# Optimization experiments

Hardware: AMD Instinct MI355X
Metric: run time of the kernel (lower is better)

Reference implementation:

```python
import jax, jax.numpy as jnp
import numpy as np


def setup_inputs() -> dict:
    key = jax.random.key(0)
    k1, k2, k3 = jax.random.split(key, 3)
    bs, nvars, T, input_dim = 8, 16, 512, 256
    embed_dim, num_embed, codebook_num = 128, 512, 4
    inp = jax.random.normal(k1, (bs, nvars, T, input_dim), dtype=jnp.float32)
    # xavier_normal_ for (input_dim, embed_dim): std = sqrt(2/(fan_in+fan_out))
    xavier_std = float(np.sqrt(2.0 / (input_dim + embed_dim)))
    projector = jax.random.normal(k2, (input_dim, embed_dim), dtype=jnp.float32) * xavier_std
    codebook = jax.random.normal(k3, (codebook_num, num_embed, embed_dim), dtype=jnp.float32)
    return {"input": inp, "projector": projector, "codebook": codebook}


def reference(input, projector, codebook):
    # project: [b,n,t,input_dim] @ [input_dim,embed_dim] -> [b,n,t,d]
    x = jnp.matmul(input, projector)
    # L2-normalize along last dim (matches torch .norm(dim=-1,keepdim=True) division)
    x = x / jnp.linalg.norm(x, axis=-1, keepdims=True)
    cb = codebook / jnp.linalg.norm(codebook, axis=-1, keepdims=True)
    # cosine similarity: [b,n,t,c,m]
    similarity = jnp.einsum('bntd,cmd->bntcm', x, cb)
    # nearest code per codebook: [b,n,t,c]
    idx = jnp.argmax(similarity, axis=-1)
    return idx
```

## Files before the change

### kernel.cpp

```cpp
#include <hip/hip_runtime.h>
#include <math.h>

#define DIN    256
#define DEMB   128
#define NCB    4
#define MCODES 512
#define NCODE  2048
#define MARGIN 1.5e-4f

using bf16x8 = __attribute__((ext_vector_type(8))) short;
using f32x16 = __attribute__((ext_vector_type(16))) float;

static __device__ __forceinline__ unsigned short f2bf(float f) {
    unsigned u = __float_as_uint(f);
    u += 0x7FFFu + ((u >> 16) & 1u);
    return (unsigned short)(u >> 16);
}
static __device__ __forceinline__ float bf2f(unsigned short h) {
    return __uint_as_float(((unsigned)h) << 16);
}
static __device__ __forceinline__ float4 ld4(const float* p) {
    return *reinterpret_cast<const float4*>(p);
}
static __device__ __forceinline__ void gload_lds16(const void* g, void* l) {
    __builtin_amdgcn_global_load_lds(
        (const __attribute__((address_space(1))) void*)g,
        (__attribute__((address_space(3))) void*)l, 16, 0, 0);
}

__global__ __launch_bounds__(256) void prep_codebook(
        const float* __restrict__ cb, float* __restrict__ cbn,
        unsigned short* __restrict__ cbA) {
    const int w = threadIdx.x >> 6, lane = threadIdx.x & 63;
    const int code = blockIdx.x * 4 + w;
    const float2 v = reinterpret_cast<const float2*>(cb + (size_t)code * DEMB)[lane];
    float ss = v.x * v.x + v.y * v.y;
#pragma unroll
    for (int m = 1; m < 64; m <<= 1) ss += __shfl_xor(ss, m, 64);
    const float rn = 1.0f / sqrtf(ss);
    const float x0 = v.x * rn, x1 = v.y * rn;
    reinterpret_cast<float2*>(cbn + (size_t)code * DEMB)[lane] = make_float2(x0, x1);

    const unsigned short h0 = f2bf(x0), h1 = f2bf(x1);
    const unsigned short l0 = f2bf(x0 - bf2f(h0)), l1 = f2bf(x1 - bf2f(h1));
    const int ct = code >> 5, ci = code & 31;
    const int kt = lane >> 3, g = (lane >> 2) & 1, i = 2 * (lane & 3);
    const size_t base = ((size_t)ct * 1024 + kt * 128 + g * 32 + ci) * 8 + i;
    *reinterpret_cast<ushort2*>(cbA + base)       = make_ushort2(h0, h1);
    *reinterpret_cast<ushort2*>(cbA + base + 512) = make_ushort2(l0, l1);
}

__global__ __launch_bounds__(256) void prep_proj(
        const float* __restrict__ proj, unsigned short* __restrict__ pjA) {
    const int t = blockIdx.x * 256 + threadIdx.x;
    const int ci = t & 31, g = (t >> 5) & 1, kt = (t >> 6) & 15, mt = t >> 10;
    const int m = mt * 32 + ci;
    const size_t base = ((size_t)(mt * 16 + kt) * 3) * 512 + (size_t)(g * 32 + ci) * 8;
#pragma unroll
    for (int i = 0; i < 8; ++i) {
        const float v = proj[(size_t)(kt * 16 + g * 8 + i) * DEMB + m];
        const unsigned short h = f2bf(v);
        const float r1 = v - bf2f(h);
        const unsigned short md = f2bf(r1);
        const float r2 = r1 - bf2f(md);
        pjA[base + i]        = h;
        pjA[base + 512 + i]  = md;
        pjA[base + 1024 + i] = f2bf(r2);
    }
}

__global__ __launch_bounds__(256) void project_mfma(
        const float* __restrict__ inp, const unsigned short* __restrict__ pjA,
        float* __restrict__ xw) {
    const int tid = threadIdx.x;
    const int lane = tid & 63, mt = tid >> 6, kg = lane >> 5;
    const int row = blockIdx.x * 32 + (lane & 31);
    const float* xr = inp + (size_t)row * DIN;
    const unsigned short* pL = pjA + (size_t)lane * 8;

    auto ldin = [&](float4& a, float4& b, int kt) {
        a = ld4(xr + kt * 16 + kg * 8);
        b = ld4(xr + kt * 16 + kg * 8 + 4);
    };

    f32x16 P, Q;
#pragma unroll
    for (int r = 0; r < 16; ++r) { P[r] = 0.0f; Q[r] = 0.0f; }

    auto do_step = [&](const float4& c0, const float4& c1, int kt) {
        const float xs[8] = {c0.x, c0.y, c0.z, c0.w, c1.x, c1.y, c1.z, c1.w};
        bf16x8 Bh, Bm, Bl;
#pragma unroll
        for (int e = 0; e < 8; ++e) {
            const float v = xs[e];
            const unsigned short h = f2bf(v);
            const float r1 = v - bf2f(h);
            const unsigned short md = f2bf(r1);
            const float r2 = r1 - bf2f(md);
            Bh[e] = (short)h; Bm[e] = (short)md; Bl[e] = (short)f2bf(r2);
        }
        const unsigned short* pf = pL + ((size_t)(mt * 16 + kt) * 3) * 512;
        const bf16x8 Ah = *reinterpret_cast<const bf16x8*>(pf);
        const bf16x8 Am = *reinterpret_cast<const bf16x8*>(pf + 512);
        const bf16x8 Al = *reinterpret_cast<const bf16x8*>(pf + 1024);
        P = __builtin_amdgcn_mfma_f32_32x32x16_bf16(Ah, Bh, P, 0, 0, 0);
        Q = __builtin_amdgcn_mfma_f32_32x32x16_bf16(Ah, Bm, Q, 0, 0, 0);
        Q = __builtin_amdgcn_mfma_f32_32x32x16_bf16(Am, Bh, Q, 0, 0, 0);
        Q = __builtin_amdgcn_mfma_f32_32x32x16_bf16(Ah, Bl, Q, 0, 0, 0);
        Q = __builtin_amdgcn_mfma_f32_32x32x16_bf16(Al, Bh, Q, 0, 0, 0);
        Q = __builtin_amdgcn_mfma_f32_32x32x16_bf16(Am, Bm, Q, 0, 0, 0);
    };

    float4 nA0, nA1, nB0, nB1;
    ldin(nA0, nA1, 0);
#pragma unroll 1
    for (int kt = 0; kt < 16; kt += 2) {
        ldin(nB0, nB1, kt + 1);
        do_step(nA0, nA1, kt);
        if (kt + 2 < 16) ldin(nA0, nA1, kt + 2);
        do_step(nB0, nB1, kt + 1);
    }

#pragma unroll
    for (int q = 0; q < 4; ++q) {
        float4 v;
        v.x = P[q * 4 + 0] + Q[q * 4 + 0];
        v.y = P[q * 4 + 1] + Q[q * 4 + 1];
        v.z = P[q * 4 + 2] + Q[q * 4 + 2];
        v.w = P[q * 4 + 3] + Q[q * 4 + 3];
        *reinterpret_cast<float4*>(xw + (size_t)row * DEMB + mt * 32 + q * 8 + kg * 4) = v;
    }
}

__global__ __launch_bounds__(256) void project_kernel(
        const float* __restrict__ inp, const float* __restrict__ proj,
        float* __restrict__ xw) {
    const int tid = threadIdx.x, tx = tid & 31, ty = tid >> 5;
    const int rowBase = blockIdx.x * 64;

    float acc1[8][4];
#pragma unroll
    for (int i = 0; i < 8; ++i)
#pragma unroll
        for (int j = 0; j < 4; ++j) acc1[i][j] = 0.0f;

    const float* inRow0 = inp + (size_t)(rowBase + ty) * DIN;
    const float* pjCol  = proj + tx * 4;

    float4 ivA[8], ivB[8], pjA[4], pjB[4];
    auto load_step = [&](float4 iv[8], float4 pj[4], int kk) {
#pragma unroll
        for (int j = 0; j < 4; ++j) pj[j] = ld4(pjCol + (size_t)(kk + j) * DEMB);
#pragma unroll
        for (int i = 0; i < 8; ++i) iv[i] = ld4(inRow0 + (size_t)(8 * i) * DIN + kk);
    };
    auto fma_step = [&](const float4 iv[8], const float4 pj[4]) {
#pragma unroll
        for (int i = 0; i < 8; ++i) {
            const float* ivp = reinterpret_cast<const float*>(&iv[i]);
#pragma unroll
            for (int j = 0; j < 4; ++j) {
                acc1[i][0] = fmaf(ivp[j], pj[j].x, acc1[i][0]);
                acc1[i][1] = fmaf(ivp[j], pj[j].y, acc1[i][1]);
                acc1[i][2] = fmaf(ivp[j], pj[j].z, acc1[i][2]);
                acc1[i][3] = fmaf(ivp[j], pj[j].w, acc1[i][3]);
            }
        }
    };
    load_step(ivA, pjA, 0);
#pragma unroll 1
    for (int k = 0; k < DIN; k += 8) {
        load_step(ivB, pjB, k + 4);
        fma_step(ivA, pjA);
        if (k + 8 < DIN) load_step(ivA, pjA, k + 8);
        fma_step(ivB, pjB);
    }
#pragma unroll
    for (int i = 0; i < 8; ++i) {
        const int r = rowBase + ty + 8 * i;
        *reinterpret_cast<float4*>(xw + (size_t)r * DEMB + tx * 4) =
            make_float4(acc1[i][0], acc1[i][1], acc1[i][2], acc1[i][3]);
    }
}

__global__ __launch_bounds__(256) void sim_kernel(
        const float* __restrict__ xw,
        const unsigned short* __restrict__ cbA,
        int* __restrict__ out, int* __restrict__ unc_cnt,
        int* __restrict__ unc_list) {
    __shared__ __align__(16) short sA[3][8192];
    const int tid = threadIdx.x;
    const int lane = tid & 63, wv = tid >> 6;
    const int kg = lane >> 5;
    const int cbi = blockIdx.x & 3;
    const int rowBase = (blockIdx.x >> 2) * 128;
    const int row = rowBase + wv * 32 + (lane & 31);

    const short* gA = (const short*)cbA + (size_t)cbi * 16 * 8192;
    auto stage = [&](int buf, int t) {
        const short* g = gA + (size_t)t * 8192 + wv * 2048 + lane * 8;
        short* l = &sA[buf][wv * 2048];
#pragma unroll
        for (int c = 0; c < 4; ++c)
            gload_lds16(g + c * 512, l + c * 512);
    };

    stage(0, 0);
    stage(1, 1);

    bf16x8 Bhi[8], Blo[8];
    {
        const float* xr = xw + (size_t)row * DEMB;
        float4 f0[8], f1[8];
        float ss = 0.0f;
#pragma unroll
        for (int kt = 0; kt < 8; ++kt) {
            f0[kt] = ld4(xr + kt * 16 + kg * 8);
            f1[kt] = ld4(xr + kt * 16 + kg * 8 + 4);
            ss += f0[kt].x * f0[kt].x + f0[kt].y * f0[kt].y +
                  f0[kt].z * f0[kt].z + f0[kt].w * f0[kt].w +
                  f1[kt].x * f1[kt].x + f1[kt].y * f1[kt].y +
                  f1[kt].z * f1[kt].z + f1[kt].w * f1[kt].w;
        }
        ss += __shfl_xor(ss, 32, 64);
        const float rn = 1.0f / sqrtf(ss);
#pragma unroll
        for (int kt = 0; kt < 8; ++kt) {
            const float xs[8] = {f0[kt].x, f0[kt].y, f0[kt].z, f0[kt].w,
                                 f1[kt].x, f1[kt].y, f1[kt].z, f1[kt].w};
            bf16x8 hv, lv;
#pragma unroll
            for (int e = 0; e < 8; ++e) {
                const float xn = xs[e] * rn;
                const unsigned short h = f2bf(xn);
                hv[e] = (short)h;
                lv[e] = (short)f2bf(xn - bf2f(h));
            }
            Bhi[kt] = hv; Blo[kt] = lv;
        }
    }

    f32x16 TWO;
#pragma unroll
    for (int r = 0; r < 16; ++r) TWO[r] = 2.0f;

    f32x16 acc = TWO;
    float t1 = -INFINITY, t2 = -INFINITY; int i1 = 0;

#pragma unroll 1
    for (int g = 0; g < 16; ++g) {
        if (g < 15) asm volatile("s_waitcnt vmcnt(4)" ::: "memory");
        else        asm volatile("s_waitcnt vmcnt(0)" ::: "memory");
        __builtin_amdgcn_s_barrier();
        asm volatile("" ::: "memory");
        if (g + 2 < 16) stage((g + 2) % 3, g + 2);

        const short* pa = &sA[g % 3][lane * 8];
        const f32x16 pAcc = acc;
        __builtin_amdgcn_s_setprio(1);
#pragma unroll
        for (int kt = 0; kt < 8; ++kt) {
            const bf16x8 Ahi = *reinterpret_cast<const bf16x8*>(pa + kt * 1024);
            const bf16x8 Alo = *reinterpret_cast<const bf16x8*>(pa + kt * 1024 + 512);
            acc = __builtin_amdgcn_mfma_f32_32x32x16_bf16(Ahi, Bhi[kt], kt ? acc : TWO, 0, 0, 0);
            acc = __builtin_amdgcn_mfma_f32_32x32x16_bf16(Ahi, Blo[kt], acc, 0, 0, 0);
            acc = __builtin_amdgcn_mfma_f32_32x32x16_bf16(Alo, Bhi[kt], acc, 0, 0, 0);
        }
        __builtin_amdgcn_s_setprio(0);

        if (g > 0) {
            const int base = (g - 1) * 32;
#pragma unroll
            for (int r = 0; r < 16; ++r) {
                const float v = pAcc[r];
                const int gidx = base + (r & 3) + 8 * (r >> 2) + 4 * kg;
                t2 = fmaxf(t2, fminf(v, t1));
                if (v > t1) { t1 = v; i1 = gidx; }
            }
        }
    }
    {
        const int base = 15 * 32;
#pragma unroll
        for (int r = 0; r < 16; ++r) {
            const float v = acc[r];
            const int gidx = base + (r & 3) + 8 * (r >> 2) + 4 * kg;
            t2 = fmaxf(t2, fminf(v, t1));
            if (v > t1) { t1 = v; i1 = gidx; }
        }
    }

    const float o1 = __shfl_xor(t1, 32, 64);
    const float o2 = __shfl_xor(t2, 32, 64);
    const int   oi = __shfl_xor(i1, 32, 64);
    const float m2 = fmaxf(fmaxf(t2, o2), fminf(t1, o1));
    if (o1 > t1 || (o1 == t1 && oi < i1)) { t1 = o1; i1 = oi; }
    const bool unc = (t1 - m2) < MARGIN;
    if (lane < 32 && !unc)
        out[(size_t)row * NCB + cbi] = i1;

    unsigned long long msk = __ballot(unc && lane < 32);
    if (lane == 0 && msk) {
        const int n = __popcll(msk);
        int base = atomicAdd(unc_cnt, n);
        while (msk) {
            const int r = __ffsll(msk) - 1; msk &= msk - 1;
            unc_list[base++] = ((rowBase + wv * 32 + r) << 2) | cbi;
        }
    }
}

__global__ __launch_bounds__(256) void recheck_kernel(
        const float* __restrict__ inp, const float* __restrict__ proj,
        const float* __restrict__ cbn,
        const int* __restrict__ unc_cnt, const int* __restrict__ unc_list,
        int* __restrict__ out) {
    __shared__ float sx[4][DEMB];
    const int lane = threadIdx.x & 63, wv = threadIdx.x >> 6;
    const int n = *unc_cnt;
    for (int it = blockIdx.x * 4 + wv; it < n; it += gridDim.x * 4) {
        const int item = unc_list[it];
        const int row = item >> 2, cbi = item & 3;
        {
            const float* ir = inp + (size_t)row * DIN;
            float a0 = 0.0f, a1 = 0.0f;
#pragma unroll 2
            for (int k = 0; k < DIN; k += 4) {
                const float4 iv = ld4(ir + k);
                const float* ivp = reinterpret_cast<const float*>(&iv);
#pragma unroll
                for (int j = 0; j < 4; ++j) {
                    a0 = fmaf(ivp[j], proj[(size_t)(k + j) * DEMB + lane],      a0);
                    a1 = fmaf(ivp[j], proj[(size_t)(k + j) * DEMB + lane + 64], a1);
                }
            }
            sx[wv][lane] = a0; sx[wv][lane + 64] = a1;
        }
        float best = -INFINITY; int bi = 0;
#pragma unroll 2
        for (int j = 0; j < 8; ++j) {
            const int c = lane + 64 * j;
            const float* cv = cbn + ((size_t)cbi * MCODES + c) * DEMB;
            float s0 = 0, s1 = 0, s2 = 0, s3 = 0;
#pragma unroll 4
            for (int k = 0; k < DEMB; k += 4) {
                const float4 xk = ld4(&sx[wv][k]);
                const float4 ck = ld4(cv + k);
                s0 = fmaf(xk.x, ck.x, s0); s1 = fmaf(xk.y, ck.y, s1);
                s2 = fmaf(xk.z, ck.z, s2); s3 = fmaf(xk.w, ck.w, s3);
            }
            const float s = (s0 + s1) + (s2 + s3);
            if (s > best) { best = s; bi = c; }
        }
#pragma unroll
        for (int mm = 1; mm < 64; mm <<= 1) {
            const float ov = __shfl_xor(best, mm, 64);
            const int   oc = __shfl_xor(bi, mm, 64);
            if (ov > best || (ov == best && oc < bi)) { best = ov; bi = oc; }
        }
        if (lane == 0) out[(size_t)row * NCB + cbi] = bi;
    }
}

__global__ __launch_bounds__(256) void fused_quantize_kernel(
        const float* __restrict__ inp, const float* __restrict__ proj,
        const float* __restrict__ cbn, const unsigned short* __restrict__ cbA,
        int* __restrict__ out) {
    __shared__ float sX[128][132];
    __shared__ float sRn[128];
    const int tid = threadIdx.x;
    const int tx = tid & 31, ty = tid >> 5;
    const int rowBase = blockIdx.x * 128;

#pragma unroll 1
    for (int p = 0; p < 2; ++p) {
        float acc1[8][4];
#pragma unroll
        for (int i = 0; i < 8; ++i)
#pragma unroll
            for (int j = 0; j < 4; ++j) acc1[i][j] = 0.0f;
        const float* inRow0 = inp + (size_t)(rowBase + p * 64 + ty) * DIN;
        const float* pjCol  = proj + tx * 4;
        float4 ivA[8], ivB[8], pjA[4], pjB[4];
        auto load_step = [&](float4 iv[8], float4 pj[4], int kk) {
#pragma unroll
            for (int j = 0; j < 4; ++j) pj[j] = ld4(pjCol + (size_t)(kk + j) * DEMB);
#pragma unroll
            for (int i = 0; i < 8; ++i) iv[i] = ld4(inRow0 + (size_t)(8 * i) * DIN + kk);
        };
        auto fma_step = [&](const float4 iv[8], const float4 pj[4]) {
#pragma unroll
            for (int i = 0; i < 8; ++i) {
                const float* ivp = reinterpret_cast<const float*>(&iv[i]);
#pragma unroll
                for (int j = 0; j < 4; ++j) {
                    acc1[i][0] = fmaf(ivp[j], pj[j].x, acc1[i][0]);
                    acc1[i][1] = fmaf(ivp[j], pj[j].y, acc1[i][1]);
                    acc1[i][2] = fmaf(ivp[j], pj[j].z, acc1[i][2]);
                    acc1[i][3] = fmaf(ivp[j], pj[j].w, acc1[i][3]);
                }
            }
        };
        load_step(ivA, pjA, 0);
#pragma unroll 1
        for (int k = 0; k < DIN; k += 8) {
            load_step(ivB, pjB, k + 4);
            fma_step(ivA, pjA);
            if (k + 8 < DIN) load_step(ivA, pjA, k + 8);
            fma_step(ivB, pjB);
        }
#pragma unroll
        for (int i = 0; i < 8; ++i) {
            const int r = p * 64 + ty + 8 * i;
            float ss = acc1[i][0] * acc1[i][0] + acc1[i][1] * acc1[i][1] +
                       acc1[i][2] * acc1[i][2] + acc1[i][3] * acc1[i][3];
#pragma unroll
            for (int mm = 1; mm < 32; mm <<= 1) ss += __shfl_xor(ss, mm, 64);
            if (tx == 0) sRn[r] = 1.0f / sqrtf(ss);
            *reinterpret_cast<float4*>(&sX[r][tx * 4]) =
                make_float4(acc1[i][0], acc1[i][1], acc1[i][2], acc1[i][3]);
        }
    }
    __syncthreads();

    const int lane = tid & 63, wv = tid >> 6;
    const int kg = lane >> 5;
    const int rowL = wv * 32 + (lane & 31);
    bf16x8 Bhi[8], Blo[8];
    {
        const float rn = sRn[rowL];
#pragma unroll
        for (int kt = 0; kt < 8; ++kt) {
            const int k0 = kt * 16 + kg * 8;
            float4 f0 = ld4(&sX[rowL][k0]);
            float4 f1 = ld4(&sX[rowL][k0 + 4]);
            float xs[8] = {f0.x, f0.y, f0.z, f0.w, f1.x, f1.y, f1.z, f1.w};
            bf16x8 hv, lv;
#pragma unroll
            for (int e = 0; e < 8; ++e) {
                const float xn = xs[e] * rn;
                const unsigned short h = f2bf(xn);
                hv[e] = (short)h;
                lv[e] = (short)f2bf(xn - bf2f(h));
            }
            Bhi[kt] = hv; Blo[kt] = lv;
        }
    }
    float t1 = -INFINITY, t2 = -INFINITY; int i1 = 0;
    const short* pA = reinterpret_cast<const short*>(cbA) + (size_t)lane * 8;
#pragma unroll 1
    for (int ct = 0; ct < 64; ++ct) {
        if ((ct & 1) == 0) __syncthreads();
        const short* pct = pA + (size_t)ct * 8192;
        f32x16 accA, accB;
#pragma unroll
        for (int r = 0; r < 16; ++r) { accA[r] = 0.0f; accB[r] = 0.0f; }
#pragma unroll
        for (int kt = 0; kt < 8; ++kt) {
            const bf16x8 Ahi = *reinterpret_cast<const bf16x8*>(pct + kt * 1024);
            const bf16x8 Alo = *reinterpret_cast<const bf16x8*>(pct + kt * 1024 + 512);
            accA = __builtin_amdgcn_mfma_f32_32x32x16_bf16(Ahi, Bhi[kt], accA, 0, 0, 0);
            accB = __builtin_amdgcn_mfma_f32_32x32x16_bf16(Ahi, Blo[kt], accB, 0, 0, 0);
            accB = __builtin_amdgcn_mfma_f32_32x32x16_bf16(Alo, Bhi[kt], accB, 0, 0, 0);
        }
#pragma unroll
        for (int r = 0; r < 16; ++r) {
            const float v = accA[r] + accB[r];
            const int gidx = ct * 32 + ((r & 3) + 8 * (r >> 2) + 4 * kg);
            t2 = fmaxf(t2, fminf(v, t1));
            if (v > t1) { t1 = v; i1 = gidx; }
        }
        if ((ct & 15) == 15) {
            const int cbi = ct >> 4;
            const float o1 = __shfl_xor(t1, 32, 64);
            const float o2 = __shfl_xor(t2, 32, 64);
            const int   oi = __shfl_xor(i1, 32, 64);
            const float m2 = fmaxf(fmaxf(t2, o2), fminf(t1, o1));
            if (o1 > t1 || (o1 == t1 && oi < i1)) { t1 = o1; i1 = oi; }
            const bool unc = (t1 - m2) < MARGIN;
            if (lane < 32 && !unc)
                out[(size_t)(rowBase + rowL) * NCB + cbi] = i1 - cbi * MCODES;
            unsigned long long msk = __ballot(unc && lane < 32);
            while (msk) {
                const int r = __ffsll(msk) - 1; msk &= msk - 1;
                const int rl = wv * 32 + r;
                float best = -INFINITY; int bi = 0;
#pragma unroll 1
                for (int j = 0; j < 8; ++j) {
                    const int c = lane + 64 * j;
                    const float* cv = cbn + ((size_t)cbi * MCODES + c) * DEMB;
                    float s0 = 0, s1 = 0, s2 = 0, s3 = 0;
#pragma unroll
                    for (int k = 0; k < DEMB; k += 4) {
                        const float4 xk = ld4(&sX[rl][k]);
                        const float4 ck = ld4(cv + k);
                        s0 = fmaf(xk.x, ck.x, s0); s1 = fmaf(xk.y, ck.y, s1);
                        s2 = fmaf(xk.z, ck.z, s2); s3 = fmaf(xk.w, ck.w, s3);
                    }
                    const float s = (s0 + s1) + (s2 + s3);
                    if (s > best) { best = s; bi = c; }
                }
#pragma unroll
                for (int mm = 1; mm < 64; mm <<= 1) {
                    const float ov = __shfl_xor(best, mm, 64);
                    const int   oc = __shfl_xor(bi, mm, 64);
                    if (ov > best || (ov == best && oc < bi)) { best = ov; bi = oc; }
                }
                if (lane == 0) out[(size_t)(rowBase + rl) * NCB + cbi] = bi;
            }
            t1 = -INFINITY; t2 = -INFINITY; i1 = 0;
        }
    }
}

extern "C" void kernel_launch(void* const* d_in, const int* in_sizes, int n_in,
                              void* d_out, int out_size, void* d_ws, size_t ws_size,
                              hipStream_t stream) {
    const float* inp  = (const float*)d_in[0];
    const float* proj = (const float*)d_in[1];
    const float* cb   = (const float*)d_in[2];
    int* out = (int*)d_out;

    char* ws = (char*)d_ws;
    float* cbn = (float*)ws;
    unsigned short* cbA = (unsigned short*)(ws + (1 << 20));
    float* xw  = (float*)(ws + (2 << 20) + (1 << 18));
    const size_t off_cnt = (size_t)(2 << 20) + (1 << 18) + ((size_t)32 << 20);
    int* unc_cnt  = (int*)(ws + off_cnt);
    int* unc_list = (int*)(ws + off_cnt + 256);
    const size_t off_pjA = off_cnt + 256 + (1 << 20);
    unsigned short* pjA = (unsigned short*)(ws + off_pjA);
    const size_t need_old = off_pjA;
    const size_t need_new = off_pjA + 192 * 1024;

    hipLaunchKernelGGL(prep_codebook, dim3(NCODE / 4), dim3(256), 0, stream,
                       cb, cbn, cbA);
    if (ws_size >= need_old) {
        hipMemsetAsync(unc_cnt, 0, 4, stream);
        if (ws_size >= need_new) {
            hipLaunchKernelGGL(prep_proj, dim3(16), dim3(256), 0, stream, proj, pjA);
            hipLaunchKernelGGL(project_mfma, dim3(2048), dim3(256), 0, stream,
                               inp, pjA, xw);
        } else {
            hipLaunchKernelGGL(project_kernel, dim3(1024), dim3(256), 0, stream,
                               inp, proj, xw);
        }
        hipLaunchKernelGGL(sim_kernel, dim3(2048), dim3(256), 0, stream,
                           xw, cbA, out, unc_cnt, unc_list);
        hipLaunchKernelGGL(recheck_kernel, dim3(1024), dim3(256), 0, stream,
                           inp, proj, cbn, unc_cnt, unc_list, out);
    } else {
        hipLaunchKernelGGL(fused_quantize_kernel, dim3(512), dim3(256), 0, stream,
                           inp, proj, cbn, cbA, out);
    }
}
```

Baseline: 234.8 us.

## Prefetch projector fragments, split sim accumulators, parallelize recheck across waves

project_mfma now loads the projector bf16 fragments one step ahead together with the input, instead of loading them inside each step. sim_kernel splits the single serial MFMA accumulator chain into three independent accumulators that are summed in the epilogue, and fully unrolls the group loop. This shortens the MFMA dependency chains at the cost of more registers. recheck_kernel now gives each uncertain item to a whole block, with one wave projecting and four waves sharing the code scan, and the launch grid is doubled.

Result: faster. 219.6 us (-6.5%).

```diff
diff --git a/kernel.cpp b/kernel.cpp
--- a/kernel.cpp
+++ b/kernel.cpp
@@ -82,12 +82,19 @@
         a = ld4(xr + kt * 16 + kg * 8);
         b = ld4(xr + kt * 16 + kg * 8 + 4);
     };
+    auto ldA = [&](bf16x8& h, bf16x8& m, bf16x8& l, int kt) {
+        const unsigned short* pf = pL + ((size_t)(mt * 16 + kt) * 3) * 512;
+        h = *reinterpret_cast<const bf16x8*>(pf);
+        m = *reinterpret_cast<const bf16x8*>(pf + 512);
+        l = *reinterpret_cast<const bf16x8*>(pf + 1024);
+    };
 
     f32x16 P, Q;
 #pragma unroll
     for (int r = 0; r < 16; ++r) { P[r] = 0.0f; Q[r] = 0.0f; }
 
-    auto do_step = [&](const float4& c0, const float4& c1, int kt) {
+    auto do_step = [&](const float4& c0, const float4& c1,
+                       const bf16x8& Ah, const bf16x8& Am, const bf16x8& Al) {
         const float xs[8] = {c0.x, c0.y, c0.z, c0.w, c1.x, c1.y, c1.z, c1.w};
         bf16x8 Bh, Bm, Bl;
 #pragma unroll
@@ -99,10 +106,6 @@
             const float r2 = r1 - bf2f(md);
             Bh[e] = (short)h; Bm[e] = (short)md; Bl[e] = (short)f2bf(r2);
         }
-        const unsigned short* pf = pL + ((size_t)(mt * 16 + kt) * 3) * 512;
-        const bf16x8 Ah = *reinterpret_cast<const bf16x8*>(pf);
-        const bf16x8 Am = *reinterpret_cast<const bf16x8*>(pf + 512);
-        const bf16x8 Al = *reinterpret_cast<const bf16x8*>(pf + 1024);
         P = __builtin_amdgcn_mfma_f32_32x32x16_bf16(Ah, Bh, P, 0, 0, 0);
         Q = __builtin_amdgcn_mfma_f32_32x32x16_bf16(Ah, Bm, Q, 0, 0, 0);
         Q = __builtin_amdgcn_mfma_f32_32x32x16_bf16(Am, Bh, Q, 0, 0, 0);
@@ -111,14 +114,17 @@
         Q = __builtin_amdgcn_mfma_f32_32x32x16_bf16(Am, Bm, Q, 0, 0, 0);
     };
 
-    float4 nA0, nA1, nB0, nB1;
-    ldin(nA0, nA1, 0);
+    float4 iA0, iA1, iB0, iB1;
+    bf16x8 hA, mA, lA, hB, mB, lB;
+    ldin(iA0, iA1, 0); ldA(hA, mA, lA, 0);
+    ldin(iB0, iB1, 1); ldA(hB, mB, lB, 1);
+
 #pragma unroll 1
     for (int kt = 0; kt < 16; kt += 2) {
-        ldin(nB0, nB1, kt + 1);
-        do_step(nA0, nA1, kt);
-        if (kt + 2 < 16) ldin(nA0, nA1, kt + 2);
-        do_step(nB0, nB1, kt + 1);
+        do_step(iA0, iA1, hA, mA, lA);
+        if (kt + 2 < 16) { ldin(iA0, iA1, kt + 2); ldA(hA, mA, lA, kt + 2); }
+        do_step(iB0, iB1, hB, mB, lB);
+        if (kt + 3 < 16) { ldin(iB0, iB1, kt + 3); ldA(hB, mB, lB, kt + 3); }
     }
 
 #pragma unroll
@@ -240,14 +246,26 @@
         }
     }
 
-    f32x16 TWO;
-#pragma unroll
-    for (int r = 0; r < 16; ++r) TWO[r] = 2.0f;
-
-    f32x16 acc = TWO;
+    f32x16 TWO, ZERO;
+#pragma unroll
+    for (int r = 0; r < 16; ++r) { TWO[r] = 2.0f; ZERO[r] = 0.0f; }
+
     float t1 = -INFINITY, t2 = -INFINITY; int i1 = 0;
-
-#pragma unroll 1
+    f32x16 cA = TWO, cB1 = ZERO, cB2 = ZERO;
+
+    auto epi = [&](const f32x16& vA, const f32x16& vB1, const f32x16& vB2,
+                   int gprev) {
+        const int base = gprev * 32;
+#pragma unroll
+        for (int r = 0; r < 16; ++r) {
+            const float v = (vA[r] + vB1[r]) + vB2[r];
+            const int gidx = base + (r & 3) + 8 * (r >> 2) + 4 * kg;
+            t2 = fmaxf(t2, fminf(v, t1));
+            if (v > t1) { t1 = v; i1 = gidx; }
+        }
+    };
+
+#pragma unroll
     for (int g = 0; g < 16; ++g) {
         if (g < 15) asm volatile("s_waitcnt vmcnt(4)" ::: "memory");
         else        asm volatile("s_waitcnt vmcnt(0)" ::: "memory");
@@ -256,39 +274,22 @@
         if (g + 2 < 16) stage((g + 2) % 3, g + 2);
 
         const short* pa = &sA[g % 3][lane * 8];
-        const f32x16 pAcc = acc;
+        f32x16 nA, nB1, nB2;
         __builtin_amdgcn_s_setprio(1);
 #pragma unroll
         for (int kt = 0; kt < 8; ++kt) {
             const bf16x8 Ahi = *reinterpret_cast<const bf16x8*>(pa + kt * 1024);
             const bf16x8 Alo = *reinterpret_cast<const bf16x8*>(pa + kt * 1024 + 512);
-            acc = __builtin_amdgcn_mfma_f32_32x32x16_bf16(Ahi, Bhi[kt], kt ? acc : TWO, 0, 0, 0);
-            acc = __builtin_amdgcn_mfma_f32_32x32x16_bf16(Ahi, Blo[kt], acc, 0, 0, 0);
-            acc = __builtin_amdgcn_mfma_f32_32x32x16_bf16(Alo, Bhi[kt], acc, 0, 0, 0);
+            nA  = __builtin_amdgcn_mfma_f32_32x32x16_bf16(Ahi, Bhi[kt], kt ? nA  : TWO,  0, 0, 0);
+            nB1 = __builtin_amdgcn_mfma_f32_32x32x16_bf16(Ahi, Blo[kt], kt ? nB1 : ZERO, 0, 0, 0);
+            nB2 = __builtin_amdgcn_mfma_f32_32x32x16_bf16(Alo, Bhi[kt], kt ? nB2 : ZERO, 0, 0, 0);
         }
         __builtin_amdgcn_s_setprio(0);
 
-        if (g > 0) {
-            const int base = (g - 1) * 32;
-#pragma unroll
-            for (int r = 0; r < 16; ++r) {
-                const float v = pAcc[r];
-                const int gidx = base + (r & 3) + 8 * (r >> 2) + 4 * kg;
-                t2 = fmaxf(t2, fminf(v, t1));
-                if (v > t1) { t1 = v; i1 = gidx; }
-            }
-        }
-    }
-    {
-        const int base = 15 * 32;
-#pragma unroll
-        for (int r = 0; r < 16; ++r) {
-            const float v = acc[r];
-            const int gidx = base + (r & 3) + 8 * (r >> 2) + 4 * kg;
-            t2 = fmaxf(t2, fminf(v, t1));
-            if (v > t1) { t1 = v; i1 = gidx; }
-        }
-    }
+        if (g > 0) epi(cA, cB1, cB2, g - 1);
+        cA = nA; cB1 = nB1; cB2 = nB2;
+    }
+    epi(cA, cB1, cB2, 15);
 
     const float o1 = __shfl_xor(t1, 32, 64);
     const float o2 = __shfl_xor(t2, 32, 64);
@@ -315,13 +316,15 @@
         const float* __restrict__ cbn,
         const int* __restrict__ unc_cnt, const int* __restrict__ unc_list,
         int* __restrict__ out) {
-    __shared__ float sx[4][DEMB];
+    __shared__ float sx[DEMB];
+    __shared__ float sBest[4];
+    __shared__ int   sIdx[4];
     const int lane = threadIdx.x & 63, wv = threadIdx.x >> 6;
     const int n = *unc_cnt;
-    for (int it = blockIdx.x * 4 + wv; it < n; it += gridDim.x * 4) {
+    for (int it = blockIdx.x; it < n; it += gridDim.x) {
         const int item = unc_list[it];
         const int row = item >> 2, cbi = item & 3;
-        {
+        if (wv == 0) {
             const float* ir = inp + (size_t)row * DIN;
             float a0 = 0.0f, a1 = 0.0f;
 #pragma unroll 2
@@ -334,17 +337,19 @@
                     a1 = fmaf(ivp[j], proj[(size_t)(k + j) * DEMB + lane + 64], a1);
                 }
             }
-            sx[wv][lane] = a0; sx[wv][lane + 64] = a1;
-        }
+            sx[lane] = a0; sx[lane + 64] = a1;
+        }
+        __syncthreads();
+
         float best = -INFINITY; int bi = 0;
-#pragma unroll 2
-        for (int j = 0; j < 8; ++j) {
-            const int c = lane + 64 * j;
+#pragma unroll
+        for (int j = 0; j < 2; ++j) {
+            const int c = wv * 128 + lane + 64 * j;
             const float* cv = cbn + ((size_t)cbi * MCODES + c) * DEMB;
             float s0 = 0, s1 = 0, s2 = 0, s3 = 0;
 #pragma unroll 4
             for (int k = 0; k < DEMB; k += 4) {
-                const float4 xk = ld4(&sx[wv][k]);
+                const float4 xk = ld4(&sx[k]);
                 const float4 ck = ld4(cv + k);
                 s0 = fmaf(xk.x, ck.x, s0); s1 = fmaf(xk.y, ck.y, s1);
                 s2 = fmaf(xk.z, ck.z, s2); s3 = fmaf(xk.w, ck.w, s3);
@@ -358,7 +363,17 @@
             const int   oc = __shfl_xor(bi, mm, 64);
             if (ov > best || (ov == best && oc < bi)) { best = ov; bi = oc; }
         }
-        if (lane == 0) out[(size_t)row * NCB + cbi] = bi;
+        if (lane == 0) { sBest[wv] = best; sIdx[wv] = bi; }
+        __syncthreads();
+        if (wv == 0 && lane == 0) {
+            float b = sBest[0]; int bidx = sIdx[0];
+#pragma unroll
+            for (int w = 1; w < 4; ++w) {
+                if (sBest[w] > b) { b = sBest[w]; bidx = sIdx[w]; }
+            }
+            out[(size_t)row * NCB + cbi] = bidx;
+        }
+        __syncthreads();
     }
 }
 
@@ -547,7 +562,7 @@
         }
         hipLaunchKernelGGL(sim_kernel, dim3(2048), dim3(256), 0, stream,
                            xw, cbA, out, unc_cnt, unc_list);
-        hipLaunchKernelGGL(recheck_kernel, dim3(1024), dim3(256), 0, stream,
+        hipLaunchKernelGGL(recheck_kernel, dim3(2048), dim3(256), 0, stream,
                            inp, proj, cbn, unc_cnt, unc_list, out);
     } else {
         hipLaunchKernelGGL(fused_quantize_kernel, dim3(512), dim3(256), 0, stream,
```
